# Optimization experiments

Hardware: AMD Instinct MI355X
Metric: run time of the kernel (lower is better)

The kernel has to match this reference:

```python
import jax, jax.numpy as jnp
import numpy as np

B, D, K, H = 8192, 1024, 4096, 8


def setup_inputs() -> dict:
    key = jax.random.key(0)
    k1, k2 = jax.random.split(key)
    inputs = jax.random.normal(k1, (B, 1, D), dtype=jnp.float32)
    # Per-head codebooks; original init decays scale by init_decay_weight**hix,
    # emulate with a 0.5**h decay so later heads model smaller residuals.
    decay = (0.5 ** jnp.arange(H, dtype=jnp.float32)).reshape(H, 1, 1)
    codebooks = jax.random.normal(k2, (H, K, D), dtype=jnp.float32) * decay
    return {"inputs": inputs, "codebooks": codebooks}


def reference(inputs, codebooks):
    """Hierarchical refinement quantizer, eval path (hard argmin selection).

    Cascade over heads: distances to codebook -> argmin -> gather embedding
    -> subtract from residual -> next head. Returns (quantized_sum, codes).
    """
    x = inputs[:, 0, :]                      # [B, D]
    resid = x
    quantized = jnp.zeros_like(x)
    codes = []
    n_heads = codebooks.shape[0]
    for h in range(n_heads):                 # fixed, small head count
        E = codebooks[h]                     # [K, D]
        # squared euclidean distances: ||r||^2 - 2 r.E^T + ||E||^2  -> [B, K]
        dist = (
            jnp.sum(resid * resid, axis=-1, keepdims=True)
            - 2.0 * jnp.einsum("bd,kd->bk", resid, E)
            + jnp.sum(E * E, axis=-1)
        )
        idx = jnp.argmin(dist, axis=-1)      # [B]
        onehot = jax.nn.one_hot(idx, E.shape[0], dtype=resid.dtype)  # [B, K]
        q = onehot @ E                       # [B, D] gathered embedding
        quantized = quantized + q
        resid = resid - q
        codes.append(idx)
    vq_codes = jnp.stack(codes, axis=1)      # [B, H]
    return quantized, vq_codes
```

## Files before the change

### kernel.cpp

```cpp
#include <hip/hip_runtime.h>

#define B_ 8192
#define D_ 1024
#define K_ 4096
#define H_ 8

#define BM 128
#define BN 128
#define BK 32
#define NBLK 64
#define NCAND 8

typedef __attribute__((ext_vector_type(8))) short short8v;
typedef __attribute__((ext_vector_type(4))) float f32x4;

#define FINF 3.4e38f
#define IBIG 0x7fffffff

__device__ __forceinline__ void amin(float& v, int& i, float v2, int i2) {
    if (v2 < v || (v2 == v && i2 < i)) { v = v2; i = i2; }
}

__device__ __forceinline__ unsigned short f2bf_rn(float x) {
    unsigned int u = __float_as_uint(x);
    unsigned int r = (u + 0x7fffu + ((u >> 16) & 1u)) >> 16;
    return (unsigned short)r;
}

__device__ __forceinline__ void gload16(const unsigned short* g, unsigned short* l) {
    __builtin_amdgcn_global_load_lds(
        (const __attribute__((address_space(1))) void*)g,
        (__attribute__((address_space(3))) void*)l, 16, 0, 0);
}

__global__ __launch_bounds__(256) void cbconv_kernel(const float* __restrict__ E,
                                                     unsigned short* __restrict__ hi,
                                                     float* __restrict__ eeh) {
    const int row = blockIdx.x;
    const int t = threadIdx.x;
    float4 v = reinterpret_cast<const float4*>(E + (size_t)row * D_)[t];
    ushort4 h;
    h.x = f2bf_rn(v.x); h.y = f2bf_rn(v.y);
    h.z = f2bf_rn(v.z); h.w = f2bf_rn(v.w);
    reinterpret_cast<ushort4*>(hi + (size_t)row * D_)[t] = h;
    float s = v.x * v.x + v.y * v.y + v.z * v.z + v.w * v.w;
    #pragma unroll
    for (int m = 1; m < 64; m <<= 1) s += __shfl_xor(s, m);
    __shared__ float ls[4];
    if ((t & 63) == 0) ls[t >> 6] = s;
    __syncthreads();
    if (t == 0) eeh[row] = (ls[0] + ls[1]) + (ls[2] + ls[3]);
}

__global__ __launch_bounds__(256) void init_kernel(const float* __restrict__ x,
                                                   float* __restrict__ resid,
                                                   float* __restrict__ rr,
                                                   unsigned short* __restrict__ rhi) {
    const int b = blockIdx.x;
    const int t = threadIdx.x;
    float4 v = reinterpret_cast<const float4*>(x + (size_t)b * D_)[t];
    reinterpret_cast<float4*>(resid + (size_t)b * D_)[t] = v;
    ushort4 h;
    h.x = f2bf_rn(v.x); h.y = f2bf_rn(v.y);
    h.z = f2bf_rn(v.z); h.w = f2bf_rn(v.w);
    reinterpret_cast<ushort4*>(rhi + (size_t)b * D_)[t] = h;
    float s = v.x * v.x + v.y * v.y + v.z * v.z + v.w * v.w;
    #pragma unroll
    for (int m = 1; m < 64; m <<= 1) s += __shfl_xor(s, m);
    __shared__ float ls[4];
    if ((t & 63) == 0) ls[t >> 6] = s;
    __syncthreads();
    if (t == 0) rr[b] = (ls[0] + ls[1]) + (ls[2] + ls[3]);
}

__global__ __launch_bounds__(256) void score_mfma_kernel(
    const unsigned short* __restrict__ Ch,
    const unsigned short* __restrict__ Rh,
    const float* __restrict__ ee,
    float* __restrict__ pval, int* __restrict__ pidx) {
    __shared__ unsigned short lds[2][128][BK];

    const int tid = threadIdx.x;
    const int be0 = blockIdx.x * BN;
    const int br0 = blockIdx.y * BM;

    f32x4 acc[4][4];
    #pragma unroll
    for (int i = 0; i < 4; ++i)
        #pragma unroll
        for (int j = 0; j < 4; ++j)
            #pragma unroll
            for (int r = 0; r < 4; ++r) acc[i][j][r] = 0.f;

    const int srow = tid >> 2;
    const int sch  = (tid & 3) * 8;
    const size_t rstep = (size_t)64 * D_;
    const unsigned short* pC = Ch + (size_t)(be0 + srow) * D_ + sch;
    const unsigned short* pR = Rh + (size_t)(br0 + srow) * D_ + sch;

    const int l  = tid & 63;
    const int w  = tid >> 6;
    const int wr = (w >> 1) * 64;
    const int wc = (w & 1) * 64;
    const int fr = l & 15;
    const int k8 = (l >> 4) * 8;

    for (int d0 = 0; d0 < D_; d0 += BK) {
        __syncthreads();
        gload16(pC + d0,         &lds[0][srow][sch]);
        gload16(pC + rstep + d0, &lds[0][srow + 64][sch]);
        gload16(pR + d0,         &lds[1][srow][sch]);
        gload16(pR + rstep + d0, &lds[1][srow + 64][sch]);
        __syncthreads();

        short8v a_h[4], b_h[4];
        #pragma unroll
        for (int f = 0; f < 4; ++f) {
            a_h[f] = *reinterpret_cast<const short8v*>(&lds[0][wr + f * 16 + fr][k8]);
            b_h[f] = *reinterpret_cast<const short8v*>(&lds[1][wc + f * 16 + fr][k8]);
        }
        #pragma unroll
        for (int i = 0; i < 4; ++i)
            #pragma unroll
            for (int j = 0; j < 4; ++j)
                acc[i][j] = __builtin_amdgcn_mfma_f32_16x16x32_bf16(a_h[i], b_h[j], acc[i][j], 0, 0, 0);
    }

    const int g4 = (l >> 4) * 4;
    float eb[4][4];
    int ec[4][4];
    #pragma unroll
    for (int i = 0; i < 4; ++i)
        #pragma unroll
        for (int r = 0; r < 4; ++r) {
            ec[i][r] = be0 + wr + i * 16 + g4 + r;
            eb[i][r] = ee[ec[i][r]];
        }
    const int eblk = blockIdx.x * 2 + (w >> 1);

    #pragma unroll
    for (int j = 0; j < 4; ++j) {
        const int rrow = br0 + wc + j * 16 + fr;
        float b1 = FINF; int i1 = IBIG;
        float b2 = FINF; int i2 = IBIG;
        #pragma unroll
        for (int i = 0; i < 4; ++i)
            #pragma unroll
            for (int r = 0; r < 4; ++r) {
                const float s = fmaf(-2.0f, acc[i][j][r], eb[i][r]);
                const int c = ec[i][r];
                const bool lt = (s < b1) || (s == b1 && c < i1);
                const float lv = lt ? b1 : s;
                const int   li = lt ? i1 : c;
                if (lt) { b1 = s; i1 = c; }
                amin(b2, i2, lv, li);
            }
        #pragma unroll
        for (int m = 16; m < 64; m <<= 1) {
            const float o1 = __shfl_xor(b1, m); const int oi1 = __shfl_xor(i1, m);
            const float o2 = __shfl_xor(b2, m); const int oi2 = __shfl_xor(i2, m);
            const bool lt = (o1 < b1) || (o1 == b1 && oi1 < i1);
            const float lv = lt ? b1 : o1;
            const int   li = lt ? i1 : oi1;
            if (lt) { b1 = o1; i1 = oi1; }
            amin(b2, i2, o2, oi2);
            amin(b2, i2, lv, li);
        }
        if ((l >> 4) == 0) {
            const size_t base = ((size_t)rrow * NBLK + eblk) * 2;
            pval[base] = b1;     pidx[base] = i1;
            pval[base + 1] = b2; pidx[base + 1] = i2;
        }
    }
}

__global__ __launch_bounds__(256) void update_kernel(
    float* __restrict__ resid,
    const float* __restrict__ E,
    const float* __restrict__ ee,
    const float* __restrict__ pval,
    const int* __restrict__ pidx,
    float* __restrict__ rr,
    float* __restrict__ quant,
    float* __restrict__ codes,
    unsigned short* __restrict__ rhi,
    int h) {
    const int b = blockIdx.x;
    const int t = threadIdx.x;
    __shared__ int scand[NCAND];
    __shared__ float sdot[NCAND];
    __shared__ int ssel;
    __shared__ float ls[4];

    if (t < 64) {
        const size_t base = ((size_t)b * NBLK + t) * 2;
        float v0 = pval[base], v1 = pval[base + 1];
        int i0 = pidx[base], i1 = pidx[base + 1];
        #pragma unroll
        for (int r = 0; r < NCAND; ++r) {
            float av = v0; int ai = i0;
            amin(av, ai, v1, i1);
            #pragma unroll
            for (int m = 1; m < 64; m <<= 1) {
                float ov = __shfl_xor(av, m);
                int oi = __shfl_xor(ai, m);
                amin(av, ai, ov, oi);
            }
            if (ai == i0) v0 = FINF;
            if (ai == i1) v1 = FINF;
            if (t == 0) scand[r] = ai;
        }
    }
    __syncthreads();

    const int wv = t >> 6;
    const int l = t & 63;
    const float4* r4row = reinterpret_cast<const float4*>(resid + (size_t)b * D_);
    float4 rx[4];
    #pragma unroll
    for (int q = 0; q < 4; ++q) rx[q] = r4row[q * 64 + l];

    #pragma unroll
    for (int cpass = 0; cpass < 2; ++cpass) {
        const int c = wv + cpass * 4;
        const int idx = scand[c];
        const float4* e4 = reinterpret_cast<const float4*>(E + (size_t)idx * D_);
        float dot = 0.f;
        #pragma unroll
        for (int q = 0; q < 4; ++q) {
            float4 e = e4[q * 64 + l];
            dot = fmaf(rx[q].x, e.x, dot);
            dot = fmaf(rx[q].y, e.y, dot);
            dot = fmaf(rx[q].z, e.z, dot);
            dot = fmaf(rx[q].w, e.w, dot);
        }
        #pragma unroll
        for (int m = 1; m < 64; m <<= 1) dot += __shfl_xor(dot, m);
        if (l == 0) sdot[c] = dot;
    }
    __syncthreads();

    if (t == 0) {
        const float rv = rr[b];
        float bv = FINF; int bi = IBIG;
        #pragma unroll
        for (int c = 0; c < NCAND; ++c) {
            const int idx = scand[c];
            const float s = (rv - 2.0f * sdot[c]) + ee[idx];
            amin(bv, bi, s, idx);
        }
        ssel = bi;
        codes[(size_t)b * H_ + h] = (float)bi;
    }
    __syncthreads();
    const int idx = ssel;

    const float4* q4 = reinterpret_cast<const float4*>(E + (size_t)idx * D_);
    float4* r4 = reinterpret_cast<float4*>(resid + (size_t)b * D_);
    float4* o4 = reinterpret_cast<float4*>(quant + (size_t)b * D_);

    float4 q = q4[t];
    float4 r = r4[t];
    r.x -= q.x; r.y -= q.y; r.z -= q.z; r.w -= q.w;
    r4[t] = r;

    ushort4 hh;
    hh.x = f2bf_rn(r.x); hh.y = f2bf_rn(r.y);
    hh.z = f2bf_rn(r.z); hh.w = f2bf_rn(r.w);
    reinterpret_cast<ushort4*>(rhi + (size_t)b * D_)[t] = hh;

    float4 o;
    if (h == 0) {
        o = q;
    } else {
        o = o4[t];
        o.x += q.x; o.y += q.y; o.z += q.z; o.w += q.w;
    }
    o4[t] = o;

    float s = r.x * r.x + r.y * r.y + r.z * r.z + r.w * r.w;
    #pragma unroll
    for (int m = 1; m < 64; m <<= 1) s += __shfl_xor(s, m);
    if ((t & 63) == 0) ls[t >> 6] = s;
    __syncthreads();
    if (t == 0) rr[b] = (ls[0] + ls[1]) + (ls[2] + ls[3]);
}

extern "C" void kernel_launch(void* const* d_in, const int* in_sizes, int n_in,
                              void* d_out, int out_size, void* d_ws, size_t ws_size,
                              hipStream_t stream) {
    const float* x  = (const float*)d_in[0];
    const float* cb = (const float*)d_in[1];
    float* out = (float*)d_out;
    float* quant = out;
    float* codes = out + (size_t)B_ * D_;

    char* ws = (char*)d_ws;
    size_t off = 0;
    float* resid = (float*)(ws + off); off += (size_t)B_ * D_ * 4;
    float* rr    = (float*)(ws + off); off += (size_t)B_ * 4;
    float* ee    = (float*)(ws + off); off += (size_t)H_ * K_ * 4;
    float* pval  = (float*)(ws + off); off += (size_t)B_ * NBLK * 2 * 4;
    int*   pidx  = (int*)  (ws + off); off += (size_t)B_ * NBLK * 2 * 4;
    unsigned short* rhi = (unsigned short*)(ws + off); off += (size_t)B_ * D_ * 2;
    unsigned short* chi = (unsigned short*)(ws + off); off += (size_t)K_ * D_ * 2;

    hipLaunchKernelGGL(init_kernel, dim3(B_), dim3(256), 0, stream, x, resid, rr, rhi);

    for (int h = 0; h < H_; ++h) {
        const float* E  = cb + (size_t)h * K_ * D_;
        float* eh = ee + (size_t)h * K_;
        hipLaunchKernelGGL(cbconv_kernel, dim3(K_), dim3(256), 0, stream, E, chi, eh);
        hipLaunchKernelGGL(score_mfma_kernel, dim3(K_ / BN, B_ / BM), dim3(256), 0, stream,
                           chi, rhi, eh, pval, pidx);
        hipLaunchKernelGGL(update_kernel, dim3(B_), dim3(256), 0, stream,
                           resid, E, eh, pval, pidx, rr, quant, codes, rhi, h);
    }
}
```

Measured before the change: 1.380 ms.

## Enlarge score GEMM tiles to 256x256 with double-buffered LDS, top-3 candidates

```diff
diff --git a/kernel.cpp b/kernel.cpp
--- a/kernel.cpp
+++ b/kernel.cpp
@@ -5,10 +5,8 @@
 #define K_ 4096
 #define H_ 8
 
-#define BM 128
-#define BN 128
-#define BK 32
-#define NBLK 64
+#define NBLK 32
+#define TOPB 3
 #define NCAND 8
 
 typedef __attribute__((ext_vector_type(8))) short short8v;
@@ -73,105 +71,132 @@
     if (t == 0) rr[b] = (ls[0] + ls[1]) + (ls[2] + ls[3]);
 }
 
-__global__ __launch_bounds__(256) void score_mfma_kernel(
+__global__ __launch_bounds__(512, 2) void score_mfma_kernel(
     const unsigned short* __restrict__ Ch,
     const unsigned short* __restrict__ Rh,
     const float* __restrict__ ee,
     float* __restrict__ pval, int* __restrict__ pidx) {
-    __shared__ unsigned short lds[2][128][BK];
+    __shared__ unsigned short lds[2][2][256][32];
 
     const int tid = threadIdx.x;
-    const int be0 = blockIdx.x * BN;
-    const int br0 = blockIdx.y * BM;
-
-    f32x4 acc[4][4];
-    #pragma unroll
-    for (int i = 0; i < 4; ++i)
+    const int be0 = blockIdx.x * 256;
+    const int br0 = blockIdx.y * 256;
+
+    f32x4 acc[8][4];
+    #pragma unroll
+    for (int i = 0; i < 8; ++i)
         #pragma unroll
         for (int j = 0; j < 4; ++j)
             #pragma unroll
             for (int r = 0; r < 4; ++r) acc[i][j][r] = 0.f;
 
     const int srow = tid >> 2;
-    const int sch  = (tid & 3) * 8;
-    const size_t rstep = (size_t)64 * D_;
-    const unsigned short* pC = Ch + (size_t)(be0 + srow) * D_ + sch;
-    const unsigned short* pR = Rh + (size_t)(br0 + srow) * D_ + sch;
+    const int scol = (tid & 3) * 8;
+    const unsigned short* sA0 = Ch + (size_t)(be0 + srow) * D_ + scol;
+    const unsigned short* sA1 = sA0 + (size_t)128 * D_;
+    const unsigned short* sB0 = Rh + (size_t)(br0 + srow) * D_ + scol;
+    const unsigned short* sB1 = sB0 + (size_t)128 * D_;
+    unsigned short* dbase = &lds[0][0][0][0];
+    const int dc0 = tid * 8;
+    const int dc1 = (tid + 512) * 8;
+
+    #define STAGE(p, kt) do {                                   \
+        const int _ko = (kt) * 32;                              \
+        unsigned short* _db = dbase + (p) * 16384;              \
+        gload16(sA0 + _ko, _db + dc0);                          \
+        gload16(sA1 + _ko, _db + dc1);                          \
+        gload16(sB0 + _ko, _db + 8192 + dc0);                   \
+        gload16(sB1 + _ko, _db + 8192 + dc1);                   \
+    } while (0)
 
     const int l  = tid & 63;
     const int w  = tid >> 6;
-    const int wr = (w >> 1) * 64;
-    const int wc = (w & 1) * 64;
+    const int wE = w >> 2;
+    const int wR = w & 3;
     const int fr = l & 15;
     const int k8 = (l >> 4) * 8;
 
-    for (int d0 = 0; d0 < D_; d0 += BK) {
-        __syncthreads();
-        gload16(pC + d0,         &lds[0][srow][sch]);
-        gload16(pC + rstep + d0, &lds[0][srow + 64][sch]);
-        gload16(pR + d0,         &lds[1][srow][sch]);
-        gload16(pR + rstep + d0, &lds[1][srow + 64][sch]);
-        __syncthreads();
-
-        short8v a_h[4], b_h[4];
-        #pragma unroll
-        for (int f = 0; f < 4; ++f) {
-            a_h[f] = *reinterpret_cast<const short8v*>(&lds[0][wr + f * 16 + fr][k8]);
-            b_h[f] = *reinterpret_cast<const short8v*>(&lds[1][wc + f * 16 + fr][k8]);
-        }
-        #pragma unroll
-        for (int i = 0; i < 4; ++i)
+    STAGE(0, 0);
+    for (int kt = 0; kt < 32; ++kt) {
+        const int p = kt & 1;
+        if (kt < 31) {
+            STAGE(p ^ 1, kt + 1);
+            asm volatile("s_waitcnt vmcnt(4)" ::: "memory");
+        } else {
+            asm volatile("s_waitcnt vmcnt(0)" ::: "memory");
+        }
+        __builtin_amdgcn_s_barrier();
+        __builtin_amdgcn_sched_barrier(0);
+
+        short8v af[8], bf[4];
+        #pragma unroll
+        for (int i = 0; i < 8; ++i)
+            af[i] = *reinterpret_cast<const short8v*>(&lds[p][0][wE * 128 + i * 16 + fr][k8]);
+        #pragma unroll
+        for (int j = 0; j < 4; ++j)
+            bf[j] = *reinterpret_cast<const short8v*>(&lds[p][1][wR * 64 + j * 16 + fr][k8]);
+        #pragma unroll
+        for (int i = 0; i < 8; ++i)
             #pragma unroll
             for (int j = 0; j < 4; ++j)
-                acc[i][j] = __builtin_amdgcn_mfma_f32_16x16x32_bf16(a_h[i], b_h[j], acc[i][j], 0, 0, 0);
-    }
+                acc[i][j] = __builtin_amdgcn_mfma_f32_16x16x32_bf16(af[i], bf[j], acc[i][j], 0, 0, 0);
+
+        asm volatile("s_waitcnt lgkmcnt(0)" ::: "memory");
+        __builtin_amdgcn_sched_barrier(0);
+        __builtin_amdgcn_s_barrier();
+    }
+    #undef STAGE
 
     const int g4 = (l >> 4) * 4;
-    float eb[4][4];
-    int ec[4][4];
-    #pragma unroll
-    for (int i = 0; i < 4; ++i)
+    float ev[8][4];
+    int ecd[8][4];
+    #pragma unroll
+    for (int i = 0; i < 8; ++i)
         #pragma unroll
         for (int r = 0; r < 4; ++r) {
-            ec[i][r] = be0 + wr + i * 16 + g4 + r;
-            eb[i][r] = ee[ec[i][r]];
-        }
-    const int eblk = blockIdx.x * 2 + (w >> 1);
+            ecd[i][r] = be0 + wE * 128 + i * 16 + g4 + r;
+            ev[i][r] = ee[ecd[i][r]];
+        }
+    const int eblk = blockIdx.x * 2 + wE;
+
+    #define INS3(v, c) do {                                         \
+        const float _v = (v); const int _c = (c);                   \
+        if (_v < b1 || (_v == b1 && _c < i1)) {                     \
+            b3 = b2; i3 = i2; b2 = b1; i2 = i1; b1 = _v; i1 = _c;   \
+        } else if (_v < b2 || (_v == b2 && _c < i2)) {              \
+            b3 = b2; i3 = i2; b2 = _v; i2 = _c;                     \
+        } else if (_v < b3 || (_v == b3 && _c < i3)) {              \
+            b3 = _v; i3 = _c;                                       \
+        }                                                           \
+    } while (0)
 
     #pragma unroll
     for (int j = 0; j < 4; ++j) {
-        const int rrow = br0 + wc + j * 16 + fr;
-        float b1 = FINF; int i1 = IBIG;
-        float b2 = FINF; int i2 = IBIG;
-        #pragma unroll
-        for (int i = 0; i < 4; ++i)
+        const int rrow = br0 + wR * 64 + j * 16 + fr;
+        float b1 = FINF, b2 = FINF, b3 = FINF;
+        int i1 = IBIG, i2 = IBIG, i3 = IBIG;
+        #pragma unroll
+        for (int i = 0; i < 8; ++i)
             #pragma unroll
             for (int r = 0; r < 4; ++r) {
-                const float s = fmaf(-2.0f, acc[i][j][r], eb[i][r]);
-                const int c = ec[i][r];
-                const bool lt = (s < b1) || (s == b1 && c < i1);
-                const float lv = lt ? b1 : s;
-                const int   li = lt ? i1 : c;
-                if (lt) { b1 = s; i1 = c; }
-                amin(b2, i2, lv, li);
+                const float s = fmaf(-2.0f, acc[i][j][r], ev[i][r]);
+                INS3(s, ecd[i][r]);
             }
         #pragma unroll
         for (int m = 16; m < 64; m <<= 1) {
             const float o1 = __shfl_xor(b1, m); const int oi1 = __shfl_xor(i1, m);
             const float o2 = __shfl_xor(b2, m); const int oi2 = __shfl_xor(i2, m);
-            const bool lt = (o1 < b1) || (o1 == b1 && oi1 < i1);
-            const float lv = lt ? b1 : o1;
-            const int   li = lt ? i1 : oi1;
-            if (lt) { b1 = o1; i1 = oi1; }
-            amin(b2, i2, o2, oi2);
-            amin(b2, i2, lv, li);
+            const float o3 = __shfl_xor(b3, m); const int oi3 = __shfl_xor(i3, m);
+            INS3(o1, oi1); INS3(o2, oi2); INS3(o3, oi3);
         }
         if ((l >> 4) == 0) {
-            const size_t base = ((size_t)rrow * NBLK + eblk) * 2;
+            const size_t base = ((size_t)rrow * NBLK + eblk) * TOPB;
             pval[base] = b1;     pidx[base] = i1;
             pval[base + 1] = b2; pidx[base + 1] = i2;
-        }
-    }
+            pval[base + 2] = b3; pidx[base + 2] = i3;
+        }
+    }
+    #undef INS3
 }
 
 __global__ __launch_bounds__(256) void update_kernel(
@@ -181,7 +206,6 @@
     const float* __restrict__ pval,
     const int* __restrict__ pidx,
     float* __restrict__ rr,
-    float* __restrict__ quant,
     float* __restrict__ codes,
     unsigned short* __restrict__ rhi,
     int h) {
@@ -193,13 +217,19 @@
     __shared__ float ls[4];
 
     if (t < 64) {
-        const size_t base = ((size_t)b * NBLK + t) * 2;
-        float v0 = pval[base], v1 = pval[base + 1];
-        int i0 = pidx[base], i1 = pidx[base + 1];
+        float v0 = FINF, v1 = FINF, v2 = FINF;
+        int i0 = IBIG, i1 = IBIG, i2 = IBIG;
+        if (t < NBLK) {
+            const size_t base = ((size_t)b * NBLK + t) * TOPB;
+            v0 = pval[base];     i0 = pidx[base];
+            v1 = pval[base + 1]; i1 = pidx[base + 1];
+            v2 = pval[base + 2]; i2 = pidx[base + 2];
+        }
         #pragma unroll
         for (int r = 0; r < NCAND; ++r) {
             float av = v0; int ai = i0;
             amin(av, ai, v1, i1);
+            amin(av, ai, v2, i2);
             #pragma unroll
             for (int m = 1; m < 64; m <<= 1) {
                 float ov = __shfl_xor(av, m);
@@ -208,6 +238,7 @@
             }
             if (ai == i0) v0 = FINF;
             if (ai == i1) v1 = FINF;
+            if (ai == i2) v2 = FINF;
             if (t == 0) scand[r] = ai;
         }
     }
@@ -257,7 +288,6 @@
 
     const float4* q4 = reinterpret_cast<const float4*>(E + (size_t)idx * D_);
     float4* r4 = reinterpret_cast<float4*>(resid + (size_t)b * D_);
-    float4* o4 = reinterpret_cast<float4*>(quant + (size_t)b * D_);
 
     float4 q = q4[t];
     float4 r = r4[t];
@@ -269,21 +299,25 @@
     hh.z = f2bf_rn(r.z); hh.w = f2bf_rn(r.w);
     reinterpret_cast<ushort4*>(rhi + (size_t)b * D_)[t] = hh;
 
-    float4 o;
-    if (h == 0) {
-        o = q;
-    } else {
-        o = o4[t];
-        o.x += q.x; o.y += q.y; o.z += q.z; o.w += q.w;
-    }
-    o4[t] = o;
-
     float s = r.x * r.x + r.y * r.y + r.z * r.z + r.w * r.w;
     #pragma unroll
     for (int m = 1; m < 64; m <<= 1) s += __shfl_xor(s, m);
     if ((t & 63) == 0) ls[t >> 6] = s;
     __syncthreads();
     if (t == 0) rr[b] = (ls[0] + ls[1]) + (ls[2] + ls[3]);
+}
+
+__global__ __launch_bounds__(256) void quant_kernel(const float* __restrict__ x,
+                                                    const float* __restrict__ resid,
+                                                    float* __restrict__ quant) {
+    const int b = blockIdx.x;
+    const int t = threadIdx.x;
+    float4 xv = reinterpret_cast<const float4*>(x + (size_t)b * D_)[t];
+    float4 rv = reinterpret_cast<const float4*>(resid + (size_t)b * D_)[t];
+    float4 o;
+    o.x = xv.x - rv.x; o.y = xv.y - rv.y;
+    o.z = xv.z - rv.z; o.w = xv.w - rv.w;
+    reinterpret_cast<float4*>(quant + (size_t)b * D_)[t] = o;
 }
 
 extern "C" void kernel_launch(void* const* d_in, const int* in_sizes, int n_in,
@@ -300,8 +334,8 @@
     float* resid = (float*)(ws + off); off += (size_t)B_ * D_ * 4;
     float* rr    = (float*)(ws + off); off += (size_t)B_ * 4;
     float* ee    = (float*)(ws + off); off += (size_t)H_ * K_ * 4;
-    float* pval  = (float*)(ws + off); off += (size_t)B_ * NBLK * 2 * 4;
-    int*   pidx  = (int*)  (ws + off); off += (size_t)B_ * NBLK * 2 * 4;
+    float* pval  = (float*)(ws + off); off += (size_t)B_ * NBLK * TOPB * 4;
+    int*   pidx  = (int*)  (ws + off); off += (size_t)B_ * NBLK * TOPB * 4;
     unsigned short* rhi = (unsigned short*)(ws + off); off += (size_t)B_ * D_ * 2;
     unsigned short* chi = (unsigned short*)(ws + off); off += (size_t)K_ * D_ * 2;
 
@@ -311,9 +345,10 @@
         const float* E  = cb + (size_t)h * K_ * D_;
         float* eh = ee + (size_t)h * K_;
         hipLaunchKernelGGL(cbconv_kernel, dim3(K_), dim3(256), 0, stream, E, chi, eh);
-        hipLaunchKernelGGL(score_mfma_kernel, dim3(K_ / BN, B_ / BM), dim3(256), 0, stream,
+        hipLaunchKernelGGL(score_mfma_kernel, dim3(K_ / 256, B_ / 256), dim3(512), 0, stream,
                            chi, rhi, eh, pval, pidx);
         hipLaunchKernelGGL(update_kernel, dim3(B_), dim3(256), 0, stream,
-                           resid, E, eh, pval, pidx, rr, quant, codes, rhi, h);
-    }
-}
+                           resid, E, eh, pval, pidx, rr, codes, rhi, h);
+    }
+    hipLaunchKernelGGL(quant_kernel, dim3(B_), dim3(256), 0, stream, x, resid, quant);
+}
```

Result: slower. 1.433 ms (+3.9%).

## Process one row per wavefront in update kernel and compute quantized output once at end

Applied to the files above, without the earlier changes.

```diff
diff --git a/kernel.cpp b/kernel.cpp
--- a/kernel.cpp
+++ b/kernel.cpp
@@ -9,7 +9,7 @@
 #define BN 128
 #define BK 32
 #define NBLK 64
-#define NCAND 8
+#define NCAND 6
 
 typedef __attribute__((ext_vector_type(8))) short short8v;
 typedef __attribute__((ext_vector_type(4))) float f32x4;
@@ -181,50 +181,43 @@
     const float* __restrict__ pval,
     const int* __restrict__ pidx,
     float* __restrict__ rr,
-    float* __restrict__ quant,
     float* __restrict__ codes,
     unsigned short* __restrict__ rhi,
+    const float* __restrict__ x,
+    float* __restrict__ quant,
     int h) {
-    const int b = blockIdx.x;
-    const int t = threadIdx.x;
-    __shared__ int scand[NCAND];
-    __shared__ float sdot[NCAND];
-    __shared__ int ssel;
-    __shared__ float ls[4];
-
-    if (t < 64) {
-        const size_t base = ((size_t)b * NBLK + t) * 2;
-        float v0 = pval[base], v1 = pval[base + 1];
-        int i0 = pidx[base], i1 = pidx[base + 1];
-        #pragma unroll
-        for (int r = 0; r < NCAND; ++r) {
-            float av = v0; int ai = i0;
-            amin(av, ai, v1, i1);
-            #pragma unroll
-            for (int m = 1; m < 64; m <<= 1) {
-                float ov = __shfl_xor(av, m);
-                int oi = __shfl_xor(ai, m);
-                amin(av, ai, ov, oi);
-            }
-            if (ai == i0) v0 = FINF;
-            if (ai == i1) v1 = FINF;
-            if (t == 0) scand[r] = ai;
-        }
-    }
-    __syncthreads();
-
-    const int wv = t >> 6;
-    const int l = t & 63;
+    const int w = threadIdx.x >> 6;
+    const int l = threadIdx.x & 63;
+    const int b = blockIdx.x * 4 + w;
+
+    const size_t pbase = ((size_t)b * NBLK + l) * 2;
+    float v0 = pval[pbase], v1 = pval[pbase + 1];
+    int i0 = pidx[pbase], i1 = pidx[pbase + 1];
+    int cand[NCAND];
+    #pragma unroll
+    for (int r = 0; r < NCAND; ++r) {
+        float av = v0; int ai = i0;
+        amin(av, ai, v1, i1);
+        #pragma unroll
+        for (int m = 1; m < 64; m <<= 1) {
+            float ov = __shfl_xor(av, m);
+            int oi = __shfl_xor(ai, m);
+            amin(av, ai, ov, oi);
+        }
+        if (ai == i0) v0 = FINF;
+        if (ai == i1) v1 = FINF;
+        cand[r] = ai;
+    }
+
     const float4* r4row = reinterpret_cast<const float4*>(resid + (size_t)b * D_);
     float4 rx[4];
     #pragma unroll
     for (int q = 0; q < 4; ++q) rx[q] = r4row[q * 64 + l];
 
-    #pragma unroll
-    for (int cpass = 0; cpass < 2; ++cpass) {
-        const int c = wv + cpass * 4;
-        const int idx = scand[c];
-        const float4* e4 = reinterpret_cast<const float4*>(E + (size_t)idx * D_);
+    float dots[NCAND];
+    #pragma unroll
+    for (int c = 0; c < NCAND; ++c) {
+        const float4* e4 = reinterpret_cast<const float4*>(E + (size_t)cand[c] * D_);
         float dot = 0.f;
         #pragma unroll
         for (int q = 0; q < 4; ++q) {
@@ -236,54 +229,51 @@
         }
         #pragma unroll
         for (int m = 1; m < 64; m <<= 1) dot += __shfl_xor(dot, m);
-        if (l == 0) sdot[c] = dot;
-    }
-    __syncthreads();
-
-    if (t == 0) {
-        const float rv = rr[b];
-        float bv = FINF; int bi = IBIG;
-        #pragma unroll
-        for (int c = 0; c < NCAND; ++c) {
-            const int idx = scand[c];
-            const float s = (rv - 2.0f * sdot[c]) + ee[idx];
-            amin(bv, bi, s, idx);
-        }
-        ssel = bi;
-        codes[(size_t)b * H_ + h] = (float)bi;
-    }
-    __syncthreads();
-    const int idx = ssel;
-
-    const float4* q4 = reinterpret_cast<const float4*>(E + (size_t)idx * D_);
-    float4* r4 = reinterpret_cast<float4*>(resid + (size_t)b * D_);
-    float4* o4 = reinterpret_cast<float4*>(quant + (size_t)b * D_);
-
-    float4 q = q4[t];
-    float4 r = r4[t];
-    r.x -= q.x; r.y -= q.y; r.z -= q.z; r.w -= q.w;
-    r4[t] = r;
-
-    ushort4 hh;
-    hh.x = f2bf_rn(r.x); hh.y = f2bf_rn(r.y);
-    hh.z = f2bf_rn(r.z); hh.w = f2bf_rn(r.w);
-    reinterpret_cast<ushort4*>(rhi + (size_t)b * D_)[t] = hh;
-
-    float4 o;
-    if (h == 0) {
-        o = q;
-    } else {
-        o = o4[t];
-        o.x += q.x; o.y += q.y; o.z += q.z; o.w += q.w;
-    }
-    o4[t] = o;
-
-    float s = r.x * r.x + r.y * r.y + r.z * r.z + r.w * r.w;
-    #pragma unroll
-    for (int m = 1; m < 64; m <<= 1) s += __shfl_xor(s, m);
-    if ((t & 63) == 0) ls[t >> 6] = s;
-    __syncthreads();
-    if (t == 0) rr[b] = (ls[0] + ls[1]) + (ls[2] + ls[3]);
+        dots[c] = dot;
+    }
+
+    const float rv = rr[b];
+    float bv = FINF; int bi = IBIG;
+    #pragma unroll
+    for (int c = 0; c < NCAND; ++c) {
+        const float s = (rv - 2.0f * dots[c]) + ee[cand[c]];
+        amin(bv, bi, s, cand[c]);
+    }
+    if (l == 0) codes[(size_t)b * H_ + h] = (float)bi;
+
+    const float4* q4 = reinterpret_cast<const float4*>(E + (size_t)bi * D_);
+    float4* r4w = reinterpret_cast<float4*>(resid + (size_t)b * D_);
+    ushort4* h4w = reinterpret_cast<ushort4*>(rhi + (size_t)b * D_);
+    float nrm = 0.f;
+    #pragma unroll
+    for (int q = 0; q < 4; ++q) {
+        float4 qv = q4[q * 64 + l];
+        float4 r = rx[q];
+        r.x -= qv.x; r.y -= qv.y; r.z -= qv.z; r.w -= qv.w;
+        rx[q] = r;
+        r4w[q * 64 + l] = r;
+        ushort4 hh;
+        hh.x = f2bf_rn(r.x); hh.y = f2bf_rn(r.y);
+        hh.z = f2bf_rn(r.z); hh.w = f2bf_rn(r.w);
+        h4w[q * 64 + l] = hh;
+        nrm += r.x * r.x + r.y * r.y + r.z * r.z + r.w * r.w;
+    }
+    #pragma unroll
+    for (int m = 1; m < 64; m <<= 1) nrm += __shfl_xor(nrm, m);
+    if (l == 0) rr[b] = nrm;
+
+    if (h == H_ - 1) {
+        const float4* x4 = reinterpret_cast<const float4*>(x + (size_t)b * D_);
+        float4* o4 = reinterpret_cast<float4*>(quant + (size_t)b * D_);
+        #pragma unroll
+        for (int q = 0; q < 4; ++q) {
+            float4 xv = x4[q * 64 + l];
+            float4 o;
+            o.x = xv.x - rx[q].x; o.y = xv.y - rx[q].y;
+            o.z = xv.z - rx[q].z; o.w = xv.w - rx[q].w;
+            o4[q * 64 + l] = o;
+        }
+    }
 }
 
 extern "C" void kernel_launch(void* const* d_in, const int* in_sizes, int n_in,
@@ -313,7 +303,7 @@
         hipLaunchKernelGGL(cbconv_kernel, dim3(K_), dim3(256), 0, stream, E, chi, eh);
         hipLaunchKernelGGL(score_mfma_kernel, dim3(K_ / BN, B_ / BM), dim3(256), 0, stream,
                            chi, rhi, eh, pval, pidx);
-        hipLaunchKernelGGL(update_kernel, dim3(B_), dim3(256), 0, stream,
-                           resid, E, eh, pval, pidx, rr, quant, codes, rhi, h);
-    }
-}
+        hipLaunchKernelGGL(update_kernel, dim3(B_ / 4), dim3(256), 0, stream,
+                           resid, E, eh, pval, pidx, rr, codes, rhi, x, quant, h);
+    }
+}
```

Result: faster. 1.183 ms (-14.3%).
